# Performance work log

Measured on AMD Instinct MI355X. Metric: run time of the kernel, lower is better.

The kernel has to match this reference:

```python
import jax, jax.numpy as jnp
import numpy as np

DIM = 128
K = 256
WIDTH = 0.125
POWER = 16.0
MIN_STEP = 1e-4
MAX_STEP = 0.9999
MASK_VALUE = -1e30


def setup_inputs() -> dict:
    key = jax.random.key(0)
    k1, k2, k3, k4 = jax.random.split(key, 4)
    B, L, D = 16, 4096, DIM
    s1 = 1.0 / np.sqrt(D)
    s2 = 1.0 / np.sqrt(2 * D)
    return {
        "input_seq": jax.random.normal(k1, (B, L, D), dtype=jnp.float32),
        "mask": jnp.ones((B, L), dtype=jnp.float32),
        "W1": jax.random.uniform(k2, (D, 2 * D), minval=-s1, maxval=s1, dtype=jnp.float32),
        "b1": jnp.zeros((2 * D,), dtype=jnp.float32),
        "W2": jax.random.uniform(k3, (2 * D, K - 1), minval=-s2, maxval=s2, dtype=jnp.float32),
        "Wr": jax.random.uniform(k4, (D, 1), minval=-s1, maxval=s1, dtype=jnp.float32),
        "br": jnp.zeros((1,), dtype=jnp.float32),
    }


def reference(input_seq, mask, W1, b1, W2, Wr, br):
    B, L, D = input_seq.shape
    # ---- Cal_M: attention pooling over L to produce mu: [B, K-1] ----
    attn = jnp.tanh(input_seq @ W1 + b1) @ W2              # [B, L, K-1]
    m = mask[..., None]
    attn = m * attn + (1.0 - m) * MASK_VALUE
    attn = jax.nn.softmax(attn, axis=-2)                   # softmax over L
    h = jnp.einsum('bld,blk->bkd', input_seq, attn)        # [B, K-1, D]
    mu = h @ Wr[:, 0] + br[0]                              # [B, K-1]
    # ---- TSPStepWarp: modes via softmax-cumsum, then TSP cdf ----
    n_steps = mu.shape[1]                                  # K-1
    modes = jax.nn.softmax(
        jnp.concatenate([jnp.zeros((B, 1), mu.dtype), mu], axis=1), axis=1)
    modes = jnp.cumsum(modes, axis=1)[:, :-1]              # [B, K-1]
    modes = jnp.clip(modes, MIN_STEP, MAX_STEP)
    a = jnp.clip(modes - WIDTH / 2.0, 0.0, 1.0 - WIDTH)[..., None]  # [B,K-1,1]
    b = jnp.clip(a + WIDTH, WIDTH, 1.0)
    mm = modes[..., None]                                  # [B,K-1,1]
    x = jnp.linspace(0.0, 1.0, L, dtype=mu.dtype)[None, None, :]    # [1,1,L]
    left = (mm - a) / (b - a) * jnp.clip((x - a) / (mm - a), 0.0, 1.0) ** POWER
    right = 1.0 - (b - mm) / (b - a) * jnp.clip((b - x) / (b - mm), 0.0, 1.0) ** POWER
    cdf = jnp.where(x <= mm, left, right)                  # [B, K-1, L]
    gamma = cdf.sum(axis=1) / n_steps                      # [B, L]
    original_len = n_steps + 1                             # K
    # ---- Almtx: linear-kernel soft binning, fully broadcast ----
    gamma_scaled = gamma * (original_len - 1)              # [B, L]
    ks = jnp.arange(original_len, dtype=gamma.dtype)       # [K]
    almat = jnp.maximum(1.0 - jnp.abs(gamma_scaled[..., None] - ks), 0.0)  # [B,L,K]
    return gamma_scaled, almat
```

## Files before the change

kernel.cpp:

```cpp
#include <hip/hip_runtime.h>
#include <hip/hip_bf16.h>

#define LLEN 4096
#define BATCH 16
#define NROWS 65536
#define DDIM 128
#define JDIM 256
#define KM1 255
#define BR 64
#define TPITCH 266

typedef __attribute__((ext_vector_type(8))) _Float16 h8;
typedef __attribute__((ext_vector_type(4))) _Float16 h4;
typedef __attribute__((ext_vector_type(4))) float f4v;

typedef __attribute__((address_space(3))) void lds_t;
typedef __attribute__((address_space(1))) const void gbl_t;
__device__ __forceinline__ void g2l16(const void* g, void* l) {
  __builtin_amdgcn_global_load_lds((gbl_t*)g, (lds_t*)l, 16, 0, 0);
}

__device__ __forceinline__ float clampf(float x, float lo, float hi) {
  return fminf(fmaxf(x, lo), hi);
}
__device__ __forceinline__ float tanh_fast(float x) {
  float e = __expf(2.0f * x);
  return 1.0f - 2.0f / (e + 1.0f);
}

__global__ void kW(const float* __restrict__ W1, const float* __restrict__ W2,
                   _Float16* __restrict__ W1P, _Float16* __restrict__ W2P) {
  const int T = blockIdx.x * 256 + threadIdx.x;
  if (T >= 192 * 64) return;
  const int frag = T >> 6, lane = T & 63;
  const int rr = lane & 15, g = lane >> 4;
  if (frag < 64) {
    const int jt = frag >> 2, ks = frag & 3;
    _Float16* base = W1P + (size_t)frag * 512 + lane * 8;
    #pragma unroll
    for (int i = 0; i < 8; ++i)
      base[i] = (_Float16)W1[(ks * 32 + 8 * g + i) * JDIM + jt * 16 + rr];
  } else {
    const int f2 = frag - 64;
    const int kt = f2 >> 3, ks = f2 & 7;
    const int k = kt * 16 + rr;
    _Float16* base = W2P + (size_t)f2 * 512 + lane * 8;
    #pragma unroll
    for (int i = 0; i < 8; ++i)
      base[i] = (k < KM1) ? (_Float16)W2[(ks * 32 + 8 * g + i) * KM1 + k] : (_Float16)0.0f;
  }
}

__launch_bounds__(512, 4)
__global__ void kF(const float* __restrict__ X,
                   const _Float16* __restrict__ W1P, const _Float16* __restrict__ W2P,
                   const float* __restrict__ b1, const float* __restrict__ Wr,
                   const float* __restrict__ mask,
                   float* __restrict__ partE, float* __restrict__ partR) {
  __shared__ _Float16 tS[BR * TPITCH];
  __shared__ _Float16 stg[2][8192];
  __shared__ float rS[BR];

  const int tid  = threadIdx.x;
  const int lane = tid & 63, wid = tid >> 6;
  const int rr = lane & 15, g = lane >> 4;
  const int mw = wid & 3;
  const int rw = wid >> 2;
  const int blk = blockIdx.x;
  const int b = blk >> 6;
  const int r_base = blk * BR;

  auto stage = [&](const _Float16* WP, int nsl, int ks, int buf) {
    const _Float16* g0 = WP + ((size_t)(wid * nsl + ks)) * 512 + lane * 8;
    const _Float16* g1 = WP + ((size_t)((wid + 8) * nsl + ks)) * 512 + lane * 8;
    g2l16(g0, &stg[buf][wid * 512]);
    g2l16(g1, &stg[buf][(wid + 8) * 512]);
  };

  f4v acc[4][2];
  #pragma unroll
  for (int m = 0; m < 4; ++m)
    #pragma unroll
    for (int n = 0; n < 2; ++n) { acc[m][n][0]=0.f; acc[m][n][1]=0.f; acc[m][n][2]=0.f; acc[m][n][3]=0.f; }
  float rp[2] = {0.f, 0.f};

  stage(W1P, 4, 0, 0);
  float4 xc[2][2], xn[2][2];
  #pragma unroll
  for (int nf = 0; nf < 2; ++nf) {
    const float* xp = X + (size_t)(r_base + rw * 32 + nf * 16 + rr) * DDIM + 8 * g;
    xc[nf][0] = *reinterpret_cast<const float4*>(xp);
    xc[nf][1] = *reinterpret_cast<const float4*>(xp + 4);
  }
  __syncthreads();

  #pragma unroll
  for (int ks = 0; ks < 4; ++ks) {
    if (ks < 3) {
      stage(W1P, 4, ks + 1, (ks + 1) & 1);
      #pragma unroll
      for (int nf = 0; nf < 2; ++nf) {
        const float* xp = X + (size_t)(r_base + rw * 32 + nf * 16 + rr) * DDIM + (ks + 1) * 32 + 8 * g;
        xn[nf][0] = *reinterpret_cast<const float4*>(xp);
        xn[nf][1] = *reinterpret_cast<const float4*>(xp + 4);
      }
    }
    h8 Wf[4];
    #pragma unroll
    for (int mf = 0; mf < 4; ++mf)
      Wf[mf] = *reinterpret_cast<const h8*>(&stg[ks & 1][(size_t)(mw * 4 + mf) * 512 + lane * 8]);
    h8 Bx[2];
    #pragma unroll
    for (int nf = 0; nf < 2; ++nf) {
      const float xv[8] = {xc[nf][0].x, xc[nf][0].y, xc[nf][0].z, xc[nf][0].w,
                           xc[nf][1].x, xc[nf][1].y, xc[nf][1].z, xc[nf][1].w};
      #pragma unroll
      for (int i = 0; i < 8; ++i) Bx[nf][i] = (_Float16)xv[i];
      if (mw == 0) {
        const float4 w0 = *reinterpret_cast<const float4*>(Wr + ks * 32 + 8 * g);
        const float4 w1 = *reinterpret_cast<const float4*>(Wr + ks * 32 + 8 * g + 4);
        rp[nf] += xv[0]*w0.x + xv[1]*w0.y + xv[2]*w0.z + xv[3]*w0.w
                + xv[4]*w1.x + xv[5]*w1.y + xv[6]*w1.z + xv[7]*w1.w;
      }
    }
    #pragma unroll
    for (int mf = 0; mf < 4; ++mf)
      #pragma unroll
      for (int nf = 0; nf < 2; ++nf)
        acc[mf][nf] = __builtin_amdgcn_mfma_f32_16x16x32_f16(Wf[mf], Bx[nf], acc[mf][nf], 0, 0, 0);
    if (ks < 3) {
      __syncthreads();
      #pragma unroll
      for (int nf = 0; nf < 2; ++nf) { xc[nf][0] = xn[nf][0]; xc[nf][1] = xn[nf][1]; }
    }
  }

  stage(W2P, 8, 0, 0);

  #pragma unroll
  for (int mf = 0; mf < 4; ++mf) {
    const int j0 = (mw * 4 + mf) * 16 + 4 * g;
    const float4 bv = *reinterpret_cast<const float4*>(b1 + j0);
    const float bva[4] = {bv.x, bv.y, bv.z, bv.w};
    #pragma unroll
    for (int nf = 0; nf < 2; ++nf) {
      const int rl = rw * 32 + nf * 16 + rr;
      h4 o;
      #pragma unroll
      for (int reg = 0; reg < 4; ++reg)
        o[reg] = (_Float16)tanh_fast(acc[mf][nf][reg] + bva[reg]);
      *reinterpret_cast<h4*>(&tS[rl * TPITCH + j0]) = o;
    }
  }
  if (mw == 0) {
    #pragma unroll
    for (int nf = 0; nf < 2; ++nf) {
      rp[nf] += __shfl_xor(rp[nf], 16, 64);
      rp[nf] += __shfl_xor(rp[nf], 32, 64);
    }
    if (g == 0) {
      #pragma unroll
      for (int nf = 0; nf < 2; ++nf) rS[rw * 32 + nf * 16 + rr] = rp[nf];
    }
  }
  #pragma unroll
  for (int m = 0; m < 4; ++m)
    #pragma unroll
    for (int n = 0; n < 2; ++n) { acc[m][n][0]=0.f; acc[m][n][1]=0.f; acc[m][n][2]=0.f; acc[m][n][3]=0.f; }
  __syncthreads();

  float mv[2], rv[2];
  #pragma unroll
  for (int nf = 0; nf < 2; ++nf) {
    const int rl = rw * 32 + nf * 16 + rr;
    mv[nf] = mask[r_base + rl];
    rv[nf] = rS[rl];
  }

  #pragma unroll
  for (int ks = 0; ks < 8; ++ks) {
    if (ks < 7) stage(W2P, 8, ks + 1, (ks + 1) & 1);
    h8 Wf[4];
    #pragma unroll
    for (int mf = 0; mf < 4; ++mf)
      Wf[mf] = *reinterpret_cast<const h8*>(&stg[ks & 1][(size_t)(mw * 4 + mf) * 512 + lane * 8]);
    h8 Bt[2];
    #pragma unroll
    for (int nf = 0; nf < 2; ++nf) {
      const int rl = rw * 32 + nf * 16 + rr;
      Bt[nf] = *reinterpret_cast<const h8*>(&tS[rl * TPITCH + ks * 32 + 8 * g]);
    }
    #pragma unroll
    for (int mf = 0; mf < 4; ++mf)
      #pragma unroll
      for (int nf = 0; nf < 2; ++nf)
        acc[mf][nf] = __builtin_amdgcn_mfma_f32_16x16x32_f16(Wf[mf], Bt[nf], acc[mf][nf], 0, 0, 0);
    if (ks < 7) __syncthreads();
  }

  float sE[4][4], sR[4][4];
  #pragma unroll
  for (int mf = 0; mf < 4; ++mf)
    #pragma unroll
    for (int reg = 0; reg < 4; ++reg) { sE[mf][reg] = 0.f; sR[mf][reg] = 0.f; }
  #pragma unroll
  for (int nf = 0; nf < 2; ++nf) {
    const float addm = (1.0f - mv[nf]) * (-1e30f);
    #pragma unroll
    for (int mf = 0; mf < 4; ++mf)
      #pragma unroll
      for (int reg = 0; reg < 4; ++reg) {
        const float e = __expf(mv[nf] * acc[mf][nf][reg] + addm);
        sE[mf][reg] += e;
        sR[mf][reg] += e * rv[nf];
      }
  }
  #pragma unroll
  for (int off = 1; off < 16; off <<= 1)
    #pragma unroll
    for (int mf = 0; mf < 4; ++mf)
      #pragma unroll
      for (int reg = 0; reg < 4; ++reg) {
        sE[mf][reg] += __shfl_xor(sE[mf][reg], off, 64);
        sR[mf][reg] += __shfl_xor(sR[mf][reg], off, 64);
      }
  if (rr == 0) {
    const int s = (blk & 63) * 2 + rw;
    float* pE = partE + (size_t)s * 4096 + b * 256;
    float* pR = partR + (size_t)s * 4096 + b * 256;
    #pragma unroll
    for (int mf = 0; mf < 4; ++mf)
      #pragma unroll
      for (int reg = 0; reg < 4; ++reg) {
        const int k = (mw * 4 + mf) * 16 + 4 * g + reg;
        pE[k] = sE[mf][reg];
        pR[k] = sR[mf][reg];
      }
  }
}

__global__ void kC(const float* __restrict__ partE, const float* __restrict__ partR,
                   const float* __restrict__ br, float* __restrict__ params) {
  __shared__ float red[256];
  __shared__ float sm[256];
  const int b = blockIdx.x;
  const int k = threadIdx.x;
  float v = 0.0f;
  if (k > 0) {
    const size_t idx = (size_t)b * 256 + (k - 1);
    float e0 = 0.f, e1 = 0.f, e2 = 0.f, e3 = 0.f;
    float r0 = 0.f, r1 = 0.f, r2 = 0.f, r3 = 0.f;
    #pragma unroll 4
    for (int s = 0; s < 128; s += 4) {
      e0 += partE[(size_t)(s + 0) * 4096 + idx];
      e1 += partE[(size_t)(s + 1) * 4096 + idx];
      e2 += partE[(size_t)(s + 2) * 4096 + idx];
      e3 += partE[(size_t)(s + 3) * 4096 + idx];
      r0 += partR[(size_t)(s + 0) * 4096 + idx];
      r1 += partR[(size_t)(s + 1) * 4096 + idx];
      r2 += partR[(size_t)(s + 2) * 4096 + idx];
      r3 += partR[(size_t)(s + 3) * 4096 + idx];
    }
    v = ((r0 + r1) + (r2 + r3)) / ((e0 + e1) + (e2 + e3)) + br[0];
  }
  red[k] = v; __syncthreads();
  #pragma unroll
  for (int off = 128; off > 0; off >>= 1) {
    if (k < off) red[k] = fmaxf(red[k], red[k + off]);
    __syncthreads();
  }
  const float vmax = red[0];
  __syncthreads();
  const float e = expf(v - vmax);
  red[k] = e; __syncthreads();
  #pragma unroll
  for (int off = 128; off > 0; off >>= 1) {
    if (k < off) red[k] += red[k + off];
    __syncthreads();
  }
  const float tot = red[0];
  __syncthreads();
  sm[k] = e / tot; __syncthreads();
  for (int off = 1; off < 256; off <<= 1) {
    const float add = (k >= off) ? sm[k - off] : 0.0f;
    __syncthreads();
    sm[k] += add;
    __syncthreads();
  }
  if (k < KM1) {
    const float m  = clampf(sm[k], 1e-4f, 0.9999f);
    const float a  = clampf(m - 0.0625f, 0.0f, 0.875f);
    const float bb = clampf(a + 0.125f, 0.125f, 1.0f);
    const float ba = bb - a, ma = m - a, bm = bb - m;
    float* p = params + ((size_t)b * KM1 + k) * 8;
    *reinterpret_cast<float4*>(p)     = make_float4(m, a, bb, ma / ba);
    *reinterpret_cast<float4*>(p + 4) = make_float4(1.0f / ma, bm / ba, 1.0f / bm, 0.0f);
  }
}

__launch_bounds__(256)
__global__ void kD(const float* __restrict__ params, float* __restrict__ gamma,
                   float* __restrict__ almat) {
  __shared__ float P[KM1][8];
  __shared__ float gl[128];
  __shared__ float ph[128];
  const int lc = blockIdx.x, b = blockIdx.y;
  const int tid = threadIdx.x;
  if (tid < KM1) {
    const float* p = params + ((size_t)b * KM1 + tid) * 8;
    *reinterpret_cast<float4*>(&P[tid][0]) = *reinterpret_cast<const float4*>(p);
    *reinterpret_cast<float4*>(&P[tid][4]) = *reinterpret_cast<const float4*>(p + 4);
  }
  __syncthreads();
  const int li = tid & 127, half = tid >> 7;
  const int l = lc * 128 + li;
  const float x = (float)l * (1.0f / 4095.0f);
  float gacc = 0.0f;
  const int k0 = half * 128, k1 = half ? KM1 : 128;
  for (int k = k0; k < k1; ++k) {
    const float m = P[k][0], a = P[k][1], bb = P[k][2], cL = P[k][3];
    const float iMA = P[k][4], cR = P[k][5], iBM = P[k][6];
    float u = clampf((x - a) * iMA, 0.0f, 1.0f);
    u = u * u; u = u * u; u = u * u; u = u * u;
    float w = clampf((bb - x) * iBM, 0.0f, 1.0f);
    w = w * w; w = w * w; w = w * w; w = w * w;
    const float left  = cL * u;
    const float right = 1.0f - cR * w;
    gacc += (x <= m) ? left : right;
  }
  if (half == 0) gl[li] = gacc; else ph[li] = gacc;
  __syncthreads();
  if (tid < 128) {
    const float tot = gl[tid] + ph[tid];
    gl[tid] = tot;
    gamma[(size_t)b * LLEN + lc * 128 + tid] = tot;
  }
  __syncthreads();
  const int kg = (tid & 63) * 4;
  const int i0 = tid >> 6;
  const float kg0 = (float)kg;
  const size_t base = ((size_t)b * LLEN + (size_t)lc * 128) * 256;
  for (int s = 0; s < 32; ++s) {
    const int i = s * 4 + i0;
    const float gv = gl[i];
    float4 v;
    v.x = fmaxf(1.0f - fabsf(gv - kg0), 0.0f);
    v.y = fmaxf(1.0f - fabsf(gv - (kg0 + 1.0f)), 0.0f);
    v.z = fmaxf(1.0f - fabsf(gv - (kg0 + 2.0f)), 0.0f);
    v.w = fmaxf(1.0f - fabsf(gv - (kg0 + 3.0f)), 0.0f);
    *reinterpret_cast<float4*>(&almat[base + (size_t)i * 256 + kg]) = v;
  }
}

extern "C" void kernel_launch(void* const* d_in, const int* in_sizes, int n_in,
                              void* d_out, int out_size, void* d_ws, size_t ws_size,
                              hipStream_t stream) {
  const float* X    = (const float*)d_in[0];
  const float* mask = (const float*)d_in[1];
  const float* W1   = (const float*)d_in[2];
  const float* b1   = (const float*)d_in[3];
  const float* W2   = (const float*)d_in[4];
  const float* Wr   = (const float*)d_in[5];
  const float* br   = (const float*)d_in[6];
  float* out   = (float*)d_out;
  float* gamma = out;
  float* almat = out + NROWS;
  float* partE = almat;
  float* partR = almat + (size_t)128 * 4096;
  float* params = (float*)d_ws;
  _Float16* W1P = (_Float16*)(params + (size_t)BATCH * KM1 * 8);
  _Float16* W2P = W1P + 64 * 512;

  kW<<<48, 256, 0, stream>>>(W1, W2, W1P, W2P);
  kF<<<NROWS / BR, 512, 0, stream>>>(X, W1P, W2P, b1, Wr, mask, partE, partR);
  kC<<<BATCH, 256, 0, stream>>>(partE, partR, br, params);
  kD<<<dim3(32, BATCH), 256, 0, stream>>>(params, gamma, almat);
}
```

Measured before the change: 87.32 us.

## Double rows per block, swizzle tanh LDS tile, single-buffer weight staging

Raises the fused MLP/softmax kernel's row tile from 64 to 128 rows per block, so each wave computes 4x4 MFMA fragments and every staged weight slice is reused across twice as many rows. The padded tanh tile is replaced with an XOR-swizzled 256-wide layout to avoid bank conflicts without padding. Weight staging drops from double to single buffering, and the per-row Wr projection moves from LDS to a scratch area in the gamma output. This halves the partial-sum count the combine kernel reads, but costs more registers and LDS per block, lowering occupancy, and adds extra barriers that remove load/compute overlap.

```diff
diff --git a/kernel.cpp b/kernel.cpp
--- a/kernel.cpp
+++ b/kernel.cpp
@@ -7,8 +7,7 @@
 #define DDIM 128
 #define JDIM 256
 #define KM1 255
-#define BR 64
-#define TPITCH 266
+#define BR 128
 
 typedef __attribute__((ext_vector_type(8))) _Float16 h8;
 typedef __attribute__((ext_vector_type(4))) _Float16 h4;
@@ -56,10 +55,9 @@
                    const _Float16* __restrict__ W1P, const _Float16* __restrict__ W2P,
                    const float* __restrict__ b1, const float* __restrict__ Wr,
                    const float* __restrict__ mask,
-                   float* __restrict__ partE, float* __restrict__ partR) {
-  __shared__ _Float16 tS[BR * TPITCH];
-  __shared__ _Float16 stg[2][8192];
-  __shared__ float rS[BR];
+                   float* __restrict__ rbuf, float* __restrict__ partE, float* __restrict__ partR) {
+  __shared__ _Float16 tS[BR * 256];
+  __shared__ _Float16 stgW[8192];
 
   const int tid  = threadIdx.x;
   const int lane = tid & 63, wid = tid >> 6;
@@ -67,75 +65,67 @@
   const int mw = wid & 3;
   const int rw = wid >> 2;
   const int blk = blockIdx.x;
-  const int b = blk >> 6;
+  const int b = blk >> 5;
   const int r_base = blk * BR;
 
-  auto stage = [&](const _Float16* WP, int nsl, int ks, int buf) {
-    const _Float16* g0 = WP + ((size_t)(wid * nsl + ks)) * 512 + lane * 8;
-    const _Float16* g1 = WP + ((size_t)((wid + 8) * nsl + ks)) * 512 + lane * 8;
-    g2l16(g0, &stg[buf][wid * 512]);
-    g2l16(g1, &stg[buf][(wid + 8) * 512]);
-  };
-
-  f4v acc[4][2];
+  f4v acc[4][4];
   #pragma unroll
   for (int m = 0; m < 4; ++m)
     #pragma unroll
-    for (int n = 0; n < 2; ++n) { acc[m][n][0]=0.f; acc[m][n][1]=0.f; acc[m][n][2]=0.f; acc[m][n][3]=0.f; }
-  float rp[2] = {0.f, 0.f};
-
-  stage(W1P, 4, 0, 0);
-  float4 xc[2][2], xn[2][2];
-  #pragma unroll
-  for (int nf = 0; nf < 2; ++nf) {
-    const float* xp = X + (size_t)(r_base + rw * 32 + nf * 16 + rr) * DDIM + 8 * g;
-    xc[nf][0] = *reinterpret_cast<const float4*>(xp);
-    xc[nf][1] = *reinterpret_cast<const float4*>(xp + 4);
-  }
-  __syncthreads();
+    for (int n = 0; n < 4; ++n) { acc[m][n][0]=0.f; acc[m][n][1]=0.f; acc[m][n][2]=0.f; acc[m][n][3]=0.f; }
+  float rp[4] = {0.f, 0.f, 0.f, 0.f};
 
   #pragma unroll
   for (int ks = 0; ks < 4; ++ks) {
-    if (ks < 3) {
-      stage(W1P, 4, ks + 1, (ks + 1) & 1);
-      #pragma unroll
-      for (int nf = 0; nf < 2; ++nf) {
-        const float* xp = X + (size_t)(r_base + rw * 32 + nf * 16 + rr) * DDIM + (ks + 1) * 32 + 8 * g;
-        xn[nf][0] = *reinterpret_cast<const float4*>(xp);
-        xn[nf][1] = *reinterpret_cast<const float4*>(xp + 4);
-      }
-    }
+    if (ks) __syncthreads();
+    {
+      const _Float16* g0 = W1P + (size_t)(wid * 4 + ks) * 512 + lane * 8;
+      const _Float16* g1 = W1P + (size_t)((wid + 8) * 4 + ks) * 512 + lane * 8;
+      g2l16(g0, &stgW[wid * 512]);
+      g2l16(g1, &stgW[(wid + 8) * 512]);
+    }
+    float4 xa[4], xb[4];
+    #pragma unroll
+    for (int nf = 0; nf < 4; ++nf) {
+      const float* xp = X + (size_t)(r_base + rw * 64 + nf * 16 + rr) * DDIM + ks * 32 + 8 * g;
+      xa[nf] = *reinterpret_cast<const float4*>(xp);
+      xb[nf] = *reinterpret_cast<const float4*>(xp + 4);
+    }
+    if (mw == 0) {
+      const float4 w0 = *reinterpret_cast<const float4*>(Wr + ks * 32 + 8 * g);
+      const float4 w1 = *reinterpret_cast<const float4*>(Wr + ks * 32 + 8 * g + 4);
+      #pragma unroll
+      for (int nf = 0; nf < 4; ++nf)
+        rp[nf] += xa[nf].x*w0.x + xa[nf].y*w0.y + xa[nf].z*w0.z + xa[nf].w*w0.w
+                + xb[nf].x*w1.x + xb[nf].y*w1.y + xb[nf].z*w1.z + xb[nf].w*w1.w;
+    }
+    __syncthreads();
     h8 Wf[4];
     #pragma unroll
     for (int mf = 0; mf < 4; ++mf)
-      Wf[mf] = *reinterpret_cast<const h8*>(&stg[ks & 1][(size_t)(mw * 4 + mf) * 512 + lane * 8]);
-    h8 Bx[2];
-    #pragma unroll
-    for (int nf = 0; nf < 2; ++nf) {
-      const float xv[8] = {xc[nf][0].x, xc[nf][0].y, xc[nf][0].z, xc[nf][0].w,
-                           xc[nf][1].x, xc[nf][1].y, xc[nf][1].z, xc[nf][1].w};
-      #pragma unroll
-      for (int i = 0; i < 8; ++i) Bx[nf][i] = (_Float16)xv[i];
-      if (mw == 0) {
-        const float4 w0 = *reinterpret_cast<const float4*>(Wr + ks * 32 + 8 * g);
-        const float4 w1 = *reinterpret_cast<const float4*>(Wr + ks * 32 + 8 * g + 4);
-        rp[nf] += xv[0]*w0.x + xv[1]*w0.y + xv[2]*w0.z + xv[3]*w0.w
-                + xv[4]*w1.x + xv[5]*w1.y + xv[6]*w1.z + xv[7]*w1.w;
-      }
-    }
-    #pragma unroll
-    for (int mf = 0; mf < 4; ++mf)
-      #pragma unroll
-      for (int nf = 0; nf < 2; ++nf)
+      Wf[mf] = *reinterpret_cast<const h8*>(&stgW[(mw * 4 + mf) * 512 + lane * 8]);
+    h8 Bx[4];
+    #pragma unroll
+    for (int nf = 0; nf < 4; ++nf) {
+      Bx[nf][0] = (_Float16)xa[nf].x; Bx[nf][1] = (_Float16)xa[nf].y;
+      Bx[nf][2] = (_Float16)xa[nf].z; Bx[nf][3] = (_Float16)xa[nf].w;
+      Bx[nf][4] = (_Float16)xb[nf].x; Bx[nf][5] = (_Float16)xb[nf].y;
+      Bx[nf][6] = (_Float16)xb[nf].z; Bx[nf][7] = (_Float16)xb[nf].w;
+    }
+    #pragma unroll
+    for (int mf = 0; mf < 4; ++mf)
+      #pragma unroll
+      for (int nf = 0; nf < 4; ++nf)
         acc[mf][nf] = __builtin_amdgcn_mfma_f32_16x16x32_f16(Wf[mf], Bx[nf], acc[mf][nf], 0, 0, 0);
-    if (ks < 3) {
-      __syncthreads();
-      #pragma unroll
-      for (int nf = 0; nf < 2; ++nf) { xc[nf][0] = xn[nf][0]; xc[nf][1] = xn[nf][1]; }
-    }
-  }
-
-  stage(W2P, 8, 0, 0);
+  }
+  __syncthreads();
+
+  {
+    const _Float16* g0 = W2P + (size_t)(wid * 8) * 512 + lane * 8;
+    const _Float16* g1 = W2P + (size_t)((wid + 8) * 8) * 512 + lane * 8;
+    g2l16(g0, &stgW[wid * 512]);
+    g2l16(g1, &stgW[(wid + 8) * 512]);
+  }
 
   #pragma unroll
   for (int mf = 0; mf < 4; ++mf) {
@@ -143,59 +133,67 @@
     const float4 bv = *reinterpret_cast<const float4*>(b1 + j0);
     const float bva[4] = {bv.x, bv.y, bv.z, bv.w};
     #pragma unroll
-    for (int nf = 0; nf < 2; ++nf) {
-      const int rl = rw * 32 + nf * 16 + rr;
+    for (int nf = 0; nf < 4; ++nf) {
+      const int rl = rw * 64 + nf * 16 + rr;
       h4 o;
       #pragma unroll
       for (int reg = 0; reg < 4; ++reg)
         o[reg] = (_Float16)tanh_fast(acc[mf][nf][reg] + bva[reg]);
-      *reinterpret_cast<h4*>(&tS[rl * TPITCH + j0]) = o;
+      const int idx = (rl * 256 + j0) ^ ((rl & 7) << 3);
+      *reinterpret_cast<h4*>(&tS[idx]) = o;
     }
   }
   if (mw == 0) {
     #pragma unroll
-    for (int nf = 0; nf < 2; ++nf) {
+    for (int nf = 0; nf < 4; ++nf) {
       rp[nf] += __shfl_xor(rp[nf], 16, 64);
       rp[nf] += __shfl_xor(rp[nf], 32, 64);
     }
     if (g == 0) {
       #pragma unroll
-      for (int nf = 0; nf < 2; ++nf) rS[rw * 32 + nf * 16 + rr] = rp[nf];
+      for (int nf = 0; nf < 4; ++nf)
+        rbuf[r_base + rw * 64 + nf * 16 + rr] = rp[nf];
     }
   }
   #pragma unroll
   for (int m = 0; m < 4; ++m)
     #pragma unroll
-    for (int n = 0; n < 2; ++n) { acc[m][n][0]=0.f; acc[m][n][1]=0.f; acc[m][n][2]=0.f; acc[m][n][3]=0.f; }
-  __syncthreads();
-
-  float mv[2], rv[2];
-  #pragma unroll
-  for (int nf = 0; nf < 2; ++nf) {
-    const int rl = rw * 32 + nf * 16 + rr;
+    for (int n = 0; n < 4; ++n) { acc[m][n][0]=0.f; acc[m][n][1]=0.f; acc[m][n][2]=0.f; acc[m][n][3]=0.f; }
+  __syncthreads();
+
+  float mv[4], rv[4];
+  #pragma unroll
+  for (int nf = 0; nf < 4; ++nf) {
+    const int rl = rw * 64 + nf * 16 + rr;
     mv[nf] = mask[r_base + rl];
-    rv[nf] = rS[rl];
+    rv[nf] = rbuf[r_base + rl];
   }
 
   #pragma unroll
   for (int ks = 0; ks < 8; ++ks) {
-    if (ks < 7) stage(W2P, 8, ks + 1, (ks + 1) & 1);
-    h8 Wf[4];
-    #pragma unroll
-    for (int mf = 0; mf < 4; ++mf)
-      Wf[mf] = *reinterpret_cast<const h8*>(&stg[ks & 1][(size_t)(mw * 4 + mf) * 512 + lane * 8]);
-    h8 Bt[2];
-    #pragma unroll
-    for (int nf = 0; nf < 2; ++nf) {
-      const int rl = rw * 32 + nf * 16 + rr;
-      Bt[nf] = *reinterpret_cast<const h8*>(&tS[rl * TPITCH + ks * 32 + 8 * g]);
-    }
-    #pragma unroll
-    for (int mf = 0; mf < 4; ++mf)
-      #pragma unroll
-      for (int nf = 0; nf < 2; ++nf)
+    h8 Wf[4], Bt[4];
+    #pragma unroll
+    for (int mf = 0; mf < 4; ++mf)
+      Wf[mf] = *reinterpret_cast<const h8*>(&stgW[(mw * 4 + mf) * 512 + lane * 8]);
+    #pragma unroll
+    for (int nf = 0; nf < 4; ++nf) {
+      const int rl = rw * 64 + nf * 16 + rr;
+      const int idx = (rl * 256 + ks * 32 + 8 * g) ^ ((rl & 7) << 3);
+      Bt[nf] = *reinterpret_cast<const h8*>(&tS[idx]);
+    }
+    #pragma unroll
+    for (int mf = 0; mf < 4; ++mf)
+      #pragma unroll
+      for (int nf = 0; nf < 4; ++nf)
         acc[mf][nf] = __builtin_amdgcn_mfma_f32_16x16x32_f16(Wf[mf], Bt[nf], acc[mf][nf], 0, 0, 0);
-    if (ks < 7) __syncthreads();
+    if (ks < 7) {
+      __syncthreads();
+      const _Float16* g0 = W2P + (size_t)(wid * 8 + ks + 1) * 512 + lane * 8;
+      const _Float16* g1 = W2P + (size_t)((wid + 8) * 8 + ks + 1) * 512 + lane * 8;
+      g2l16(g0, &stgW[wid * 512]);
+      g2l16(g1, &stgW[(wid + 8) * 512]);
+      __syncthreads();
+    }
   }
 
   float sE[4][4], sR[4][4];
@@ -204,7 +202,7 @@
     #pragma unroll
     for (int reg = 0; reg < 4; ++reg) { sE[mf][reg] = 0.f; sR[mf][reg] = 0.f; }
   #pragma unroll
-  for (int nf = 0; nf < 2; ++nf) {
+  for (int nf = 0; nf < 4; ++nf) {
     const float addm = (1.0f - mv[nf]) * (-1e30f);
     #pragma unroll
     for (int mf = 0; mf < 4; ++mf)
@@ -225,7 +223,7 @@
         sR[mf][reg] += __shfl_xor(sR[mf][reg], off, 64);
       }
   if (rr == 0) {
-    const int s = (blk & 63) * 2 + rw;
+    const int s = (blk & 31) * 2 + rw;
     float* pE = partE + (size_t)s * 4096 + b * 256;
     float* pR = partR + (size_t)s * 4096 + b * 256;
     #pragma unroll
@@ -251,7 +249,7 @@
     float e0 = 0.f, e1 = 0.f, e2 = 0.f, e3 = 0.f;
     float r0 = 0.f, r1 = 0.f, r2 = 0.f, r3 = 0.f;
     #pragma unroll 4
-    for (int s = 0; s < 128; s += 4) {
+    for (int s = 0; s < 64; s += 4) {
       e0 += partE[(size_t)(s + 0) * 4096 + idx];
       e1 += partE[(size_t)(s + 1) * 4096 + idx];
       e2 += partE[(size_t)(s + 2) * 4096 + idx];
@@ -365,14 +363,15 @@
   float* out   = (float*)d_out;
   float* gamma = out;
   float* almat = out + NROWS;
+  float* rbuf  = gamma;
   float* partE = almat;
-  float* partR = almat + (size_t)128 * 4096;
+  float* partR = almat + (size_t)64 * 4096;
   float* params = (float*)d_ws;
   _Float16* W1P = (_Float16*)(params + (size_t)BATCH * KM1 * 8);
   _Float16* W2P = W1P + 64 * 512;
 
   kW<<<48, 256, 0, stream>>>(W1, W2, W1P, W2P);
-  kF<<<NROWS / BR, 512, 0, stream>>>(X, W1P, W2P, b1, Wr, mask, partE, partR);
+  kF<<<NROWS / BR, 512, 0, stream>>>(X, W1P, W2P, b1, Wr, mask, rbuf, partE, partR);
   kC<<<BATCH, 256, 0, stream>>>(partE, partR, br, params);
   kD<<<dim3(32, BATCH), 256, 0, stream>>>(params, gamma, almat);
 }
```

New measurement: 86.35 us. No clear change (-1.1%).
